# Optimization experiments

Measured on AMD Instinct MI355X. Metric: run time of the kernel, lower is better.

The kernel has to match this reference:

```python
import jax, jax.numpy as jnp
import numpy as np


def setup_inputs() -> dict:
    key = jax.random.key(0)
    k1, k2, k3, k4 = jax.random.split(key, 4)
    B, T, S, D = 32, 512, 1024, 1024
    inp = jax.random.normal(k1, (B, T, D), dtype=jnp.float32)
    ctx = jax.random.normal(k2, (B, S, D), dtype=jnp.float32)
    W_in = jax.random.normal(k3, (D, D), dtype=jnp.float32) * (1.0 / np.sqrt(D))
    W_out = jax.random.normal(k4, (D, 2 * D), dtype=jnp.float32) * (1.0 / np.sqrt(2 * D))
    return {"input": inp, "context": ctx, "W_in": W_in, "W_out": W_out}


def reference(input, context, W_in, W_out):
    # GlobalAttention, attn_type='general', no mask, no coverage, tgt_len > 1.
    B, T, D = input.shape
    S = context.shape[1]
    # score: (W_in h_t) . h_s   -> [B, T, S]
    h_t = jnp.einsum('btd,ed->bte', input, W_in)           # linear_in (no bias)
    align = jnp.einsum('btd,bsd->bts', h_t, context)
    align_vectors = jax.nn.softmax(align, axis=-1)          # [B, T, S]
    # weighted sum of context
    c = jnp.einsum('bts,bsd->btd', align_vectors, context)  # [B, T, D]
    # concat [c, input] -> linear_out (no bias for 'general') -> tanh
    concat_c = jnp.concatenate([c, input], axis=-1)          # [B, T, 2D]
    attn_h = jnp.tanh(jnp.einsum('btf,df->btd', concat_c, W_out))
    # not one_step: transpose to [T, B, ...]
    attn_h = jnp.transpose(attn_h, (1, 0, 2))
    align_vectors = jnp.transpose(align_vectors, (1, 0, 2))
    return attn_h, align_vectors
```

## Files before the change

kernel.cpp:

```cpp
#include <hip/hip_runtime.h>
#include <hip/hip_bf16.h>


typedef short bf16x8 __attribute__((ext_vector_type(8)));
typedef float f32x4 __attribute__((ext_vector_type(4)));
typedef unsigned short us;

#define NB 32
#define NT 512
#define NS 1024
#define ND 1024

__device__ inline us f2bf(float x) {
  unsigned u = __float_as_uint(x);
  u += 0x7FFFu + ((u >> 16) & 1u);
  return (us)(u >> 16);
}
__device__ inline float bf2f(us h) { return __uint_as_float(((unsigned)h) << 16); }

__device__ inline void store_split(us* __restrict__ hi, us* __restrict__ lo, size_t idx, float v) {
  us h = f2bf(v);
  hi[idx] = h;
  lo[idx] = f2bf(v - bf2f(h));
}

__global__ void ga_split(const float* __restrict__ src, us* __restrict__ hi,
                         us* __restrict__ lo, long n) {
  long i0 = ((long)blockIdx.x * blockDim.x + threadIdx.x) * 4;
  long stride = (long)gridDim.x * blockDim.x * 4;
  for (long i = i0; i < n; i += stride) {
    float4 v = *reinterpret_cast<const float4*>(src + i);
    ushort4 h, l;
    h.x = f2bf(v.x); l.x = f2bf(v.x - bf2f(h.x));
    h.y = f2bf(v.y); l.y = f2bf(v.y - bf2f(h.y));
    h.z = f2bf(v.z); l.z = f2bf(v.z - bf2f(h.z));
    h.w = f2bf(v.w); l.w = f2bf(v.w - bf2f(h.w));
    *reinterpret_cast<ushort4*>(hi + i) = h;
    *reinterpret_cast<ushort4*>(lo + i) = l;
  }
}

__global__ void ga_cvt(const float* __restrict__ src, us* __restrict__ dst, long n) {
  long i0 = ((long)blockIdx.x * blockDim.x + threadIdx.x) * 4;
  long stride = (long)gridDim.x * blockDim.x * 4;
  for (long i = i0; i < n; i += stride) {
    float4 v = *reinterpret_cast<const float4*>(src + i);
    ushort4 h;
    h.x = f2bf(v.x); h.y = f2bf(v.y); h.z = f2bf(v.z); h.w = f2bf(v.w);
    *reinterpret_cast<ushort4*>(dst + i) = h;
  }
}

__global__ void ga_transpose_split(const float* __restrict__ ctx, us* __restrict__ tHi,
                                   us* __restrict__ tLo) {
  __shared__ float tile[64][65];
  int s0 = blockIdx.x << 6, d0 = blockIdx.y << 6, b = blockIdx.z;
  const float* src = ctx + (size_t)b * NS * ND;
  int tid = threadIdx.x;
#pragma unroll
  for (int i = 0; i < 16; ++i) {
    int lin = (i << 8) + tid;
    int r = lin >> 6, c = lin & 63;
    tile[r][c] = src[(size_t)(s0 + r) * ND + d0 + c];
  }
  __syncthreads();
  us* oH = tHi + (size_t)b * ND * NS;
  us* oL = tLo + (size_t)b * ND * NS;
#pragma unroll
  for (int i = 0; i < 16; ++i) {
    int lin = (i << 8) + tid;
    int dr = lin >> 6, sc = lin & 63;
    float v = tile[sc][dr];
    size_t o = (size_t)(d0 + dr) * NS + s0 + sc;
    us h = f2bf(v);
    oH[o] = h;
    oL[o] = f2bf(v - bf2f(h));
  }
}

__global__ __launch_bounds__(256) void ga_softmax(float* __restrict__ al,
                                                  us* __restrict__ pHi, us* __restrict__ pLo) {
  int row = blockIdx.x;
  int tid = threadIdx.x;
  float* p = al + (size_t)row * NS;
  float4 v = *reinterpret_cast<const float4*>(p + (tid << 2));
  float m = fmaxf(fmaxf(v.x, v.y), fmaxf(v.z, v.w));
#pragma unroll
  for (int off = 32; off; off >>= 1) m = fmaxf(m, __shfl_xor(m, off));
  __shared__ float rmax[4], rsum[4];
  int wv = tid >> 6, ln = tid & 63;
  if (ln == 0) rmax[wv] = m;
  __syncthreads();
  m = fmaxf(fmaxf(rmax[0], rmax[1]), fmaxf(rmax[2], rmax[3]));
  float4 e;
  e.x = __expf(v.x - m); e.y = __expf(v.y - m);
  e.z = __expf(v.z - m); e.w = __expf(v.w - m);
  float s = e.x + e.y + e.z + e.w;
#pragma unroll
  for (int off = 32; off; off >>= 1) s += __shfl_xor(s, off);
  if (ln == 0) rsum[wv] = s;
  __syncthreads();
  s = rsum[0] + rsum[1] + rsum[2] + rsum[3];
  float inv = 1.0f / s;
  e.x *= inv; e.y *= inv; e.z *= inv; e.w *= inv;
  *reinterpret_cast<float4*>(p + (tid << 2)) = e;
  int t = row >> 5, b = row & 31;
  size_t o = ((size_t)b * NT + t) * NS + (tid << 2);
  ushort4 h, l;
  h.x = f2bf(e.x); l.x = f2bf(e.x - bf2f(h.x));
  h.y = f2bf(e.y); l.y = f2bf(e.y - bf2f(h.y));
  h.z = f2bf(e.z); l.z = f2bf(e.z - bf2f(h.z));
  h.w = f2bf(e.w); l.w = f2bf(e.w - bf2f(h.w));
  *reinterpret_cast<ushort4*>(pHi + o) = h;
  *reinterpret_cast<ushort4*>(pLo + o) = l;
}

__device__ inline void gload16(const us* g, us* l) {
  __builtin_amdgcn_global_load_lds((const __attribute__((address_space(1))) unsigned int*)g,
                                   (__attribute__((address_space(3))) unsigned int*)l, 16, 0, 0);
}

__device__ inline void stage_plane(const us* __restrict__ src, int ld, us* __restrict__ tile, int tid) {
  int r = tid >> 3;
  int cs = (((tid & 7) ^ (r & 7)) << 3);
  const us* g = src + (size_t)r * ld + cs;
  us* l = tile + (tid << 3);
#pragma unroll
  for (int s = 0; s < 4; ++s) gload16(g + (size_t)(s * 32) * ld, l + s * 2048);
}

__device__ inline bf16x8 frag_ld(const us* tile, int row, int colb) {
  int off = (row << 7) + (colb ^ ((row & 7) << 4));
  return *reinterpret_cast<const bf16x8*>(reinterpret_cast<const char*>(tile) + off);
}

__device__ inline f32x4 mfma16(bf16x8 a, bf16x8 b, f32x4 c) {
  return __builtin_amdgcn_mfma_f32_16x16x32_bf16(a, b, c, 0, 0, 0);
}

template <int MODE>
__global__ __launch_bounds__(256, 2) void ga_gemm(
    const us* __restrict__ Ahi, const us* __restrict__ Alo,
    const us* __restrict__ A2hi, const us* __restrict__ A2lo,
    const us* __restrict__ Bhi, const us* __restrict__ Blo,
    void* __restrict__ out0, void* __restrict__ out1,
    int K, int lda, int ldb, long astride, long bstride) {
  constexpr int NTILES = (MODE == 3) ? 3 : 4;
  __shared__ __align__(16) us lds[NTILES * 8192];
  us* tAh = lds;
  us* tBh = lds + 8192;
  us* tAl = lds + 16384;
  us* tBl = (MODE == 3) ? nullptr : lds + 24576;

  int tid = threadIdx.x;
  int bx = blockIdx.x, by = blockIdx.y, bz = blockIdx.z;
  int rowA = bx * 128, colB = by * 128;

  const us* pAh = Ahi + (size_t)bz * astride + (size_t)rowA * lda;
  const us* pAl = Alo + (size_t)bz * astride + (size_t)rowA * lda;
  const us* pA2h = (MODE == 3) ? A2hi + (size_t)rowA * lda : nullptr;
  const us* pA2l = (MODE == 3) ? A2lo + (size_t)rowA * lda : nullptr;
  const us* pBh = Bhi + (size_t)bz * bstride + (size_t)colB * ldb;
  const us* pBl = (MODE == 3) ? nullptr : Blo + (size_t)bz * bstride + (size_t)colB * ldb;

  f32x4 zero = {0.f, 0.f, 0.f, 0.f};
  f32x4 acc[4][4];
#pragma unroll
  for (int m = 0; m < 4; ++m)
#pragma unroll
    for (int n = 0; n < 4; ++n) acc[m][n] = zero;

  int lane = tid & 63, wvi = tid >> 6;
  int wr = wvi >> 1, wc = wvi & 1;
  int fr = lane & 15;
  int kob = (lane >> 4) << 4;

  for (int k0 = 0; k0 < K; k0 += 64) {
    const us *sAh, *sAl;
    if constexpr (MODE == 3) {
      if (k0 < 1024) { sAh = pAh + k0; sAl = pAl + k0; }
      else           { sAh = pA2h + (k0 - 1024); sAl = pA2l + (k0 - 1024); }
    } else { sAh = pAh + k0; sAl = pAl + k0; }
    stage_plane(sAh, lda, tAh, tid);
    stage_plane(pBh + k0, ldb, tBh, tid);
    stage_plane(sAl, lda, tAl, tid);
    if constexpr (MODE != 3) stage_plane(pBl + k0, ldb, tBl, tid);
    __syncthreads();
#pragma unroll
    for (int kk = 0; kk < 2; ++kk) {
      int cb = (kk << 6) + kob;
      bf16x8 ah[4], al[4], bh[4], bl[4];
#pragma unroll
      for (int m = 0; m < 4; ++m) {
        int ra = (wr << 6) + (m << 4) + fr;
        ah[m] = frag_ld(tAh, ra, cb);
        al[m] = frag_ld(tAl, ra, cb);
      }
#pragma unroll
      for (int n = 0; n < 4; ++n) {
        int rb = (wc << 6) + (n << 4) + fr;
        bh[n] = frag_ld(tBh, rb, cb);
        if constexpr (MODE != 3) bl[n] = frag_ld(tBl, rb, cb);
      }
#pragma unroll
      for (int m = 0; m < 4; ++m)
#pragma unroll
        for (int n = 0; n < 4; ++n) {
          acc[m][n] = mfma16(ah[m], bh[n], acc[m][n]);
          if constexpr (MODE != 3) acc[m][n] = mfma16(ah[m], bl[n], acc[m][n]);
          acc[m][n] = mfma16(al[m], bh[n], acc[m][n]);
        }
    }
    __syncthreads();
  }

#pragma unroll
  for (int m = 0; m < 4; ++m)
#pragma unroll
    for (int n = 0; n < 4; ++n)
#pragma unroll
      for (int j = 0; j < 4; ++j) {
        int r = rowA + (wr << 6) + (m << 4) + ((lane >> 4) << 2) + j;
        int c = colB + (wc << 6) + (n << 4) + (lane & 15);
        float v = acc[m][n][j];
        if constexpr (MODE == 0) {
          store_split((us*)out0, (us*)out1, (size_t)r * 1024 + c, v);
        } else if constexpr (MODE == 1) {
          ((float*)out0)[((size_t)r * NB + bz) * NS + c] = v;
        } else if constexpr (MODE == 2) {
          store_split((us*)out0, (us*)out1, ((size_t)bz * NT + r) * 1024 + c, v);
        } else {
          int bb = r >> 9, tt = r & 511;
          ((float*)out0)[((size_t)tt * NB + bb) * ND + c] = tanhf(v);
        }
      }
}

extern "C" void kernel_launch(void* const* d_in, const int* in_sizes, int n_in,
                              void* d_out, int out_size, void* d_ws, size_t ws_size,
                              hipStream_t stream) {
  (void)in_sizes; (void)n_in; (void)out_size; (void)ws_size;
  const float* inp = (const float*)d_in[0];
  const float* ctx = (const float*)d_in[1];
  const float* Win = (const float*)d_in[2];
  const float* Wout = (const float*)d_in[3];
  float* out = (float*)d_out;

  char* w = (char*)d_ws;
  us* ctx_hi  = (us*)(w + 0);
  us* c_hi    = (us*)(w + 0);
  us* c_lo    = (us*)(w + 33554432);
  us* ctx_lo  = (us*)(w + 67108864);
  us* p_hi    = (us*)(w + 67108864);
  us* p_lo    = (us*)(w + 100663296);
  us* in_hi   = (us*)(w + 134217728);
  us* in_lo   = (us*)(w + 167772160);
  us* h_hi    = (us*)(w + 201326592);
  us* h_lo    = (us*)(w + 234881024);
  us* ctxT_lo = (us*)(w + 201326592);
  us* win_hi  = (us*)(w + 268435456);
  us* win_lo  = (us*)(w + 270532608);
  us* wout_b  = (us*)(w + 272629760);

  us* ctxT_hi = (us*)d_out;
  float* alignOut = out + 16777216;

  ga_split<<<2048, 256, 0, stream>>>(inp, in_hi, in_lo, 16777216L);
  ga_split<<<2048, 256, 0, stream>>>(ctx, ctx_hi, ctx_lo, 33554432L);
  ga_split<<<512, 256, 0, stream>>>(Win, win_hi, win_lo, 1048576L);
  ga_cvt<<<512, 256, 0, stream>>>(Wout, wout_b, 2097152L);

  ga_gemm<0><<<dim3(128, 8, 1), 256, 0, stream>>>(in_hi, in_lo, nullptr, nullptr,
                                                  win_hi, win_lo, h_hi, h_lo,
                                                  1024, 1024, 1024, 0L, 0L);
  ga_gemm<1><<<dim3(4, 8, 32), 256, 0, stream>>>(h_hi, h_lo, nullptr, nullptr,
                                                 ctx_hi, ctx_lo, alignOut, nullptr,
                                                 1024, 1024, 1024, 524288L, 1048576L);
  ga_transpose_split<<<dim3(16, 16, 32), 256, 0, stream>>>(ctx, ctxT_hi, ctxT_lo);
  ga_softmax<<<16384, 256, 0, stream>>>(alignOut, p_hi, p_lo);
  ga_gemm<2><<<dim3(4, 8, 32), 256, 0, stream>>>(p_hi, p_lo, nullptr, nullptr,
                                                 ctxT_hi, ctxT_lo, c_hi, c_lo,
                                                 1024, 1024, 1024, 524288L, 1048576L);
  ga_gemm<3><<<dim3(128, 8, 1), 256, 0, stream>>>(c_hi, c_lo, in_hi, in_lo,
                                                  wout_b, nullptr, out, nullptr,
                                                  2048, 1024, 2048, 0L, 0L);
}
```

Before: 637.9 us.

## Rewrite GEMM as 256x256 tile, 8-wave kernel with double-buffered async LDS pipeline

Replaces the 128x128 four-wave GEMM with a 256x256 tile kernel that uses eight waves and a 128 KB double-buffered LDS region. Global-to-LDS loads for the next K-steps are issued inside four compute phases, paced by explicit vmcnt waits and s_barrier. MFMA sections are wrapped in raised scheduling priority. The goal is to hide load latency and raise data reuse per tile, at the cost of fewer blocks, more registers and one block per CU because of the LDS footprint.

```diff
diff --git a/kernel.cpp b/kernel.cpp
--- a/kernel.cpp
+++ b/kernel.cpp
@@ -7,7 +7,7 @@
 typedef unsigned short us;
 
 #define NB 32
-#define NT 512
+#define NT_ 512
 #define NS 1024
 #define ND 1024
 
@@ -105,7 +105,7 @@
   e.x *= inv; e.y *= inv; e.z *= inv; e.w *= inv;
   *reinterpret_cast<float4*>(p + (tid << 2)) = e;
   int t = row >> 5, b = row & 31;
-  size_t o = ((size_t)b * NT + t) * NS + (tid << 2);
+  size_t o = ((size_t)b * NT_ + t) * NS + (tid << 2);
   ushort4 h, l;
   h.x = f2bf(e.x); l.x = f2bf(e.x - bf2f(h.x));
   h.y = f2bf(e.y); l.y = f2bf(e.y - bf2f(h.y));
@@ -115,46 +115,87 @@
   *reinterpret_cast<ushort4*>(pLo + o) = l;
 }
 
-__device__ inline void gload16(const us* g, us* l) {
+__device__ inline void gload16(const us* g, void* l) {
   __builtin_amdgcn_global_load_lds((const __attribute__((address_space(1))) unsigned int*)g,
                                    (__attribute__((address_space(3))) unsigned int*)l, 16, 0, 0);
 }
 
-__device__ inline void stage_plane(const us* __restrict__ src, int ld, us* __restrict__ tile, int tid) {
-  int r = tid >> 3;
-  int cs = (((tid & 7) ^ (r & 7)) << 3);
-  const us* g = src + (size_t)r * ld + cs;
-  us* l = tile + (tid << 3);
-#pragma unroll
-  for (int s = 0; s < 4; ++s) gload16(g + (size_t)(s * 32) * ld, l + s * 2048);
-}
-
-__device__ inline bf16x8 frag_ld(const us* tile, int row, int colb) {
-  int off = (row << 7) + (colb ^ ((row & 7) << 4));
-  return *reinterpret_cast<const bf16x8*>(reinterpret_cast<const char*>(tile) + off);
-}
-
 __device__ inline f32x4 mfma16(bf16x8 a, bf16x8 b, f32x4 c) {
   return __builtin_amdgcn_mfma_f32_16x16x32_bf16(a, b, c, 0, 0, 0);
 }
 
+
+#define STAGE_A(tt, q) do {                                                        \
+    const us *sah_, *sal_;                                                         \
+    if constexpr (MODE == 3) {                                                     \
+      if ((tt) < (NT >> 1)) { sah_ = pAh + (size_t)(tt) * 32;                      \
+                              sal_ = pAl + (size_t)(tt) * 32; }                    \
+      else { sah_ = pA2h + (size_t)((tt) - (NT >> 1)) * 32;                        \
+             sal_ = pA2l + (size_t)((tt) - (NT >> 1)) * 32; }                      \
+    } else { sah_ = pAh + (size_t)(tt) * 32; sal_ = pAl + (size_t)(tt) * 32; }     \
+    long so_ = aoff0 + (long)(q) * 64 * lda;                                       \
+    char* d_ = lb + (((tt) & 1) << 16) + ((q) << 13) + sdst;                       \
+    gload16(sah_ + so_, d_);                                                       \
+    gload16(sal_ + so_, d_ + 16384);                                               \
+  } while (0)
+
+#define STAGE_B(tt, q) do {                                                        \
+    long so_ = boff0 + (long)(q) * 32 * ldb + (long)(tt) * 32;                     \
+    char* d_ = lb + (((tt) & 1) << 16) + 32768 + ((q) << 13) + sdst;               \
+    gload16(pBh + so_, d_);                                                        \
+    if constexpr (MODE != 3) gload16(pBl + so_, d_ + 16384);                       \
+  } while (0)
+
+#define PHASE(QM, QN, STAGE, TAIL) do {                                            \
+    const char* pA_ = lb + (cur << 16) + ((QM) << 13);                             \
+    const char* pB_ = lb + (cur << 16) + 32768 + ((QN) << 13);                     \
+    bf16x8 ah_[4], al_[4], bh_[2], bl_[2];                                         \
+    _Pragma("unroll") for (int m = 0; m < 4; ++m) {                                \
+      ah_[m] = *(const bf16x8*)(pA_ + arb + (m << 10));                            \
+      al_[m] = *(const bf16x8*)(pA_ + 16384 + arb + (m << 10));                    \
+    }                                                                              \
+    _Pragma("unroll") for (int n = 0; n < 2; ++n) {                                \
+      bh_[n] = *(const bf16x8*)(pB_ + brb + (n << 10));                            \
+      if constexpr (MODE != 3)                                                     \
+        bl_[n] = *(const bf16x8*)(pB_ + 16384 + brb + (n << 10));                  \
+    }                                                                              \
+    STAGE;                                                                         \
+    __builtin_amdgcn_s_barrier();                                                  \
+    __builtin_amdgcn_s_setprio(1);                                                 \
+    _Pragma("unroll") for (int m = 0; m < 4; ++m)                                  \
+    _Pragma("unroll") for (int n = 0; n < 2; ++n) {                                \
+      f32x4& a_ = acc[(QM) * 4 + m][(QN) * 2 + n];                                 \
+      a_ = mfma16(ah_[m], bh_[n], a_);                                             \
+      if constexpr (MODE != 3) a_ = mfma16(ah_[m], bl_[n], a_);                    \
+      a_ = mfma16(al_[m], bh_[n], a_);                                             \
+    }                                                                              \
+    __builtin_amdgcn_s_setprio(0);                                                 \
+    TAIL;                                                                          \
+    __builtin_amdgcn_s_barrier();                                                  \
+  } while (0)
+
+#define VM_STEADY do {                                                             \
+    if constexpr (MODE == 3) asm volatile("s_waitcnt vmcnt(3)" ::: "memory");      \
+    else asm volatile("s_waitcnt vmcnt(4)" ::: "memory");                          \
+  } while (0)
+
 template <int MODE>
-__global__ __launch_bounds__(256, 2) void ga_gemm(
+__global__ __launch_bounds__(512, 2) void ga_gemm8(
     const us* __restrict__ Ahi, const us* __restrict__ Alo,
     const us* __restrict__ A2hi, const us* __restrict__ A2lo,
     const us* __restrict__ Bhi, const us* __restrict__ Blo,
     void* __restrict__ out0, void* __restrict__ out1,
     int K, int lda, int ldb, long astride, long bstride) {
-  constexpr int NTILES = (MODE == 3) ? 3 : 4;
-  __shared__ __align__(16) us lds[NTILES * 8192];
-  us* tAh = lds;
-  us* tBh = lds + 8192;
-  us* tAl = lds + 16384;
-  us* tBl = (MODE == 3) ? nullptr : lds + 24576;
-
-  int tid = threadIdx.x;
-  int bx = blockIdx.x, by = blockIdx.y, bz = blockIdx.z;
-  int rowA = bx * 128, colB = by * 128;
+  __shared__ __align__(16) char lds[131072];
+  const int NT = K >> 5;
+  const int tid = threadIdx.x;
+  const int lane = tid & 63;
+  const int wv = tid >> 6;
+  const int wr = wv >> 2, wc = wv & 3;
+  const int fr = lane & 15;
+  const int blk0 = lane >> 4;
+  const int bx = blockIdx.x, by = blockIdx.y, bz = blockIdx.z;
+  const int rowA = bx << 8, colB = by << 8;
 
   const us* pAh = Ahi + (size_t)bz * astride + (size_t)rowA * lda;
   const us* pAl = Alo + (size_t)bz * astride + (size_t)rowA * lda;
@@ -163,75 +204,59 @@
   const us* pBh = Bhi + (size_t)bz * bstride + (size_t)colB * ldb;
   const us* pBl = (MODE == 3) ? nullptr : Blo + (size_t)bz * bstride + (size_t)colB * ldb;
 
+  const int sprow = tid >> 2;
+  const int sblkx = ((tid & 3) ^ ((sprow >> 1) & 3)) << 3;
+  const long aoff0 = (long)((sprow >> 6) * 128 + (sprow & 63)) * lda + sblkx;
+  const long boff0 = (long)((sprow >> 5) * 64 + (sprow & 31)) * ldb + sblkx;
+  char* lb = lds;
+  const int sdst = tid << 4;
+
+  const int rdsw = (blk0 ^ ((fr >> 1) & 3)) << 4;
+  const int arb = (wr << 12) + (fr << 6) + rdsw;
+  const int brb = (wc << 11) + (fr << 6) + rdsw;
+
   f32x4 zero = {0.f, 0.f, 0.f, 0.f};
-  f32x4 acc[4][4];
-#pragma unroll
-  for (int m = 0; m < 4; ++m)
-#pragma unroll
-    for (int n = 0; n < 4; ++n) acc[m][n] = zero;
-
-  int lane = tid & 63, wvi = tid >> 6;
-  int wr = wvi >> 1, wc = wvi & 1;
-  int fr = lane & 15;
-  int kob = (lane >> 4) << 4;
-
-  for (int k0 = 0; k0 < K; k0 += 64) {
-    const us *sAh, *sAl;
-    if constexpr (MODE == 3) {
-      if (k0 < 1024) { sAh = pAh + k0; sAl = pAl + k0; }
-      else           { sAh = pA2h + (k0 - 1024); sAl = pA2l + (k0 - 1024); }
-    } else { sAh = pAh + k0; sAl = pAl + k0; }
-    stage_plane(sAh, lda, tAh, tid);
-    stage_plane(pBh + k0, ldb, tBh, tid);
-    stage_plane(sAl, lda, tAl, tid);
-    if constexpr (MODE != 3) stage_plane(pBl + k0, ldb, tBl, tid);
-    __syncthreads();
-#pragma unroll
-    for (int kk = 0; kk < 2; ++kk) {
-      int cb = (kk << 6) + kob;
-      bf16x8 ah[4], al[4], bh[4], bl[4];
-#pragma unroll
-      for (int m = 0; m < 4; ++m) {
-        int ra = (wr << 6) + (m << 4) + fr;
-        ah[m] = frag_ld(tAh, ra, cb);
-        al[m] = frag_ld(tAl, ra, cb);
-      }
-#pragma unroll
-      for (int n = 0; n < 4; ++n) {
-        int rb = (wc << 6) + (n << 4) + fr;
-        bh[n] = frag_ld(tBh, rb, cb);
-        if constexpr (MODE != 3) bl[n] = frag_ld(tBl, rb, cb);
-      }
-#pragma unroll
-      for (int m = 0; m < 4; ++m)
-#pragma unroll
-        for (int n = 0; n < 4; ++n) {
-          acc[m][n] = mfma16(ah[m], bh[n], acc[m][n]);
-          if constexpr (MODE != 3) acc[m][n] = mfma16(ah[m], bl[n], acc[m][n]);
-          acc[m][n] = mfma16(al[m], bh[n], acc[m][n]);
-        }
-    }
-    __syncthreads();
-  }
-
-#pragma unroll
-  for (int m = 0; m < 4; ++m)
-#pragma unroll
-    for (int n = 0; n < 4; ++n)
+  f32x4 acc[8][4];
+#pragma unroll
+  for (int i = 0; i < 8; ++i)
+#pragma unroll
+    for (int k = 0; k < 4; ++k) acc[i][k] = zero;
+
+  STAGE_A(0, 0); STAGE_B(0, 0); STAGE_A(0, 1); STAGE_B(0, 1);
+  STAGE_A(1, 0); STAGE_B(1, 0);
+  VM_STEADY;
+  __builtin_amdgcn_s_barrier();
+
+  int cur = 0;
+  for (int t = 0; t < NT; ++t) {
+    const bool s1 = (t + 1 < NT), s2 = (t + 2 < NT);
+    PHASE(0, 0, { if (s1) STAGE_A(t + 1, 1); }, {});
+    PHASE(0, 1, { if (s1) STAGE_B(t + 1, 1); }, {});
+    PHASE(1, 0, { if (s2) STAGE_A(t + 2, 0); }, {});
+    PHASE(1, 1, { if (s2) STAGE_B(t + 2, 0); },
+          { if (s1) { if (s2) { VM_STEADY; }
+                      else { asm volatile("s_waitcnt vmcnt(0)" ::: "memory"); } } });
+    cur ^= 1;
+  }
+
+#pragma unroll
+  for (int i = 0; i < 8; ++i)
+#pragma unroll
+    for (int k = 0; k < 4; ++k)
 #pragma unroll
       for (int j = 0; j < 4; ++j) {
-        int r = rowA + (wr << 6) + (m << 4) + ((lane >> 4) << 2) + j;
-        int c = colB + (wc << 6) + (n << 4) + (lane & 15);
-        float v = acc[m][n][j];
+        int r = rowA + (wr << 7) + ((i >> 2) << 6) + ((i & 3) << 4) + ((lane >> 4) << 2) + j;
+        int c = colB + (wc << 6) + ((k >> 1) << 5) + ((k & 1) << 4) + fr;
+        float v = acc[i][k][j];
         if constexpr (MODE == 0) {
           store_split((us*)out0, (us*)out1, (size_t)r * 1024 + c, v);
         } else if constexpr (MODE == 1) {
           ((float*)out0)[((size_t)r * NB + bz) * NS + c] = v;
         } else if constexpr (MODE == 2) {
-          store_split((us*)out0, (us*)out1, ((size_t)bz * NT + r) * 1024 + c, v);
+          store_split((us*)out0, (us*)out1, ((size_t)bz * 512 + r) * 1024 + c, v);
         } else {
-          int bb = r >> 9, tt = r & 511;
-          ((float*)out0)[((size_t)tt * NB + bb) * ND + c] = tanhf(v);
+          int bb = r >> 9, tt2 = r & 511;
+          ((float*)out0)[((size_t)tt2 * NB + bb) * ND + c] = tanhf(v);
         }
       }
 }
@@ -270,18 +295,18 @@
   ga_split<<<512, 256, 0, stream>>>(Win, win_hi, win_lo, 1048576L);
   ga_cvt<<<512, 256, 0, stream>>>(Wout, wout_b, 2097152L);
 
-  ga_gemm<0><<<dim3(128, 8, 1), 256, 0, stream>>>(in_hi, in_lo, nullptr, nullptr,
+  ga_gemm8<0><<<dim3(64, 4, 1), 512, 0, stream>>>(in_hi, in_lo, nullptr, nullptr,
                                                   win_hi, win_lo, h_hi, h_lo,
                                                   1024, 1024, 1024, 0L, 0L);
-  ga_gemm<1><<<dim3(4, 8, 32), 256, 0, stream>>>(h_hi, h_lo, nullptr, nullptr,
-                                                 ctx_hi, ctx_lo, alignOut, nullptr,
-                                                 1024, 1024, 1024, 524288L, 1048576L);
+  ga_gemm8<1><<<dim3(2, 4, 32), 512, 0, stream>>>(h_hi, h_lo, nullptr, nullptr,
+                                                  ctx_hi, ctx_lo, alignOut, nullptr,
+                                                  1024, 1024, 1024, 524288L, 1048576L);
   ga_transpose_split<<<dim3(16, 16, 32), 256, 0, stream>>>(ctx, ctxT_hi, ctxT_lo);
   ga_softmax<<<16384, 256, 0, stream>>>(alignOut, p_hi, p_lo);
-  ga_gemm<2><<<dim3(4, 8, 32), 256, 0, stream>>>(p_hi, p_lo, nullptr, nullptr,
-                                                 ctxT_hi, ctxT_lo, c_hi, c_lo,
-                                                 1024, 1024, 1024, 524288L, 1048576L);
-  ga_gemm<3><<<dim3(128, 8, 1), 256, 0, stream>>>(c_hi, c_lo, in_hi, in_lo,
+  ga_gemm8<2><<<dim3(2, 4, 32), 512, 0, stream>>>(p_hi, p_lo, nullptr, nullptr,
+                                                  ctxT_hi, ctxT_lo, c_hi, c_lo,
+                                                  1024, 1024, 1024, 524288L, 1048576L);
+  ga_gemm8<3><<<dim3(64, 4, 1), 512, 0, stream>>>(c_hi, c_lo, in_hi, in_lo,
                                                   wout_b, nullptr, out, nullptr,
                                                   2048, 1024, 2048, 0L, 0L);
 }
```

Result: slower. 661.6 us (+3.7%).
